# Performance work log

Hardware: AMD Instinct MI355X
Metric: run time of the kernel (lower is better)

## Reference

```python
import jax, jax.numpy as jnp
import numpy as np

# Module hyperparameters (match init_kwargs)
T0, Z0, T1, Z1, K, S, ROUTING = 4, 16, 8, 16, 5, 1, 3
PAD = 2  # hard-coded padding=2 in the torch module
N, H, W_SP = 4, 128, 128


def setup_inputs() -> dict:
    key = jax.random.key(0)
    k1, k2 = jax.random.split(key)
    u = jax.random.normal(k1, (N, T0, Z0, H, W_SP), dtype=jnp.float32)
    # t_0 independent Conv2d(z_0 -> t_1*z_1, k, s, padding=2, bias=False) weights
    W = jax.random.normal(k2, (T0, T1 * Z1, Z0, K, K), dtype=jnp.float32) * 0.05
    return {"u": u, "W": W}


def _squash(p):
    # squash along last (z_1) axis, matching torch: p_norm = sqrt(|p|^2 + 1e-9)
    n2 = jnp.sum(p * p, axis=-1, keepdims=True)
    n = jnp.sqrt(n2 + 1e-9)
    return n2 / (1.0 + n2) * p / n


def _capsule_convs(u, W):
    # t_0 independent convs == one grouped conv with feature_group_count=t_0
    n, t0, z0, h, w = u.shape
    x = u.reshape(n, t0 * z0, h, w)
    wk = W.reshape(t0 * T1 * Z1, z0, K, K)
    y = jax.lax.conv_general_dilated(
        x, wk, window_strides=(S, S), padding=[(PAD, PAD), (PAD, PAD)],
        dimension_numbers=("NCHW", "OIHW", "NCHW"), feature_group_count=t0)
    h1, w1 = y.shape[2], y.shape[3]
    # [N, t0*t1*z1, H1, W1] -> u_hat [t0, N, H1, W1, t1, z1]
    y = y.reshape(n, t0, T1, Z1, h1, w1)
    return jnp.transpose(y, (1, 0, 4, 5, 2, 3))


def _routing(u_hat):
    t0, n, h, w, t1, z1 = u_hat.shape
    dt = u_hat.dtype
    b = jnp.zeros((t0, n, t1, h, w), dt)  # NCHW layout per capsule type
    neg_inf = jnp.array(-jnp.inf, dt)
    zero = jnp.array(0.0, dt)
    win = (1, 1, 1, K, K)
    ones = (1, 1, 1, 1, 1)
    pad = [(0, 0), (0, 0), (0, 0), (PAD, PAD), (PAD, PAD)]
    v = None
    for d in range(ROUTING):
        uh = jax.lax.stop_gradient(u_hat) if d < ROUTING - 1 else u_hat
        # stability max: max_pool2d(k,1,pad=2) (pads with -inf) then max over t1
        b_max = jax.lax.reduce_window(b, neg_inf, jax.lax.max, win, ones, pad)
        b_max = jnp.max(b_max, axis=2, keepdims=True)
        c = jnp.exp(b - b_max)  # [t0, N, t1, H, W]
        # conv2d_same with ones kernel [1,t1,k,k] == channel-sum then kxk box-sum
        sum_c = jax.lax.reduce_window(jnp.sum(c, axis=2, keepdims=True), zero,
                                      jax.lax.add, win, ones, pad)
        r = c / sum_c                                   # [t0, N, t1, H, W]
        r = jnp.transpose(r, (0, 1, 3, 4, 2))[..., None]  # [t0,N,H,W,t1,1]
        p = jnp.sum(r * uh, axis=0)                     # [N, H, W, t1, z1]
        v = _squash(p)
        # NOTE: the original torch code computes b + (u_hat*v).sum(4) into a
        # list `b_t_list_` that is never assigned back, so b stays zero across
        # iterations. We faithfully reproduce that (no b update).
    return jnp.transpose(v, (0, 3, 4, 1, 2))  # [N, t1, z1, H, W]


def reference(u, W):
    return _routing(_capsule_convs(u, W))
```

## Files before the change

kernel.cpp:

```cpp
#include <hip/hip_runtime.h>
#include <hip/hip_bf16.h>


#define CO 128

typedef __attribute__((ext_vector_type(8))) short bf16x8;
typedef __attribute__((ext_vector_type(4))) float f32x4;

__device__ __forceinline__ void glds16(const void* g, void* l) {
    __builtin_amdgcn_global_load_lds((const __attribute__((address_space(1))) void*)g,
                                     (__attribute__((address_space(3))) void*)l, 16, 0, 0);
}

__global__ __launch_bounds__(256) void k_prep(const float* __restrict__ u,
                                              const float* __restrict__ Wsrc,
                                              ushort* __restrict__ ut,
                                              ushort* __restrict__ Wr2) {
    __shared__ float lt[64][65];
    int b = blockIdx.x;
    int t = threadIdx.x;
    if (b < 800) {
        int idx = b * 256 + t;
        int ci = idx & 63;
        int r  = idx >> 6;
        int co = r & 127;
        int kk = r >> 7;
        int t0 = ci >> 4, z0 = ci & 15;
        __hip_bfloat16 bb = __float2bfloat16(Wsrc[((t0 * CO + co) * 16 + z0) * 25 + kk]);
        int chunk = (ci >> 3) ^ (co & 7);
        Wr2[((kk * CO + co) << 6) + (chunk << 3) + (ci & 7)] = *(ushort*)&bb;
        return;
    }
    b -= 800;
    int wc = b & 1; int nh = b >> 1; int h = nh & 127; int n = nh >> 7;
    int w0 = wc * 64;
    int ciL = t >> 4;
    int wl  = (t & 15) * 4;
    const float* up = u + (size_t)n * (64 * 128 * 128) + h * 128 + w0;
#pragma unroll
    for (int p = 0; p < 4; ++p) {
        int ci = p * 16 + ciL;
        float4 v = *(const float4*)(up + (size_t)ci * 16384 + wl);
        lt[wl + 0][ci] = v.x;
        lt[wl + 1][ci] = v.y;
        lt[wl + 2][ci] = v.z;
        lt[wl + 3][ci] = v.w;
    }
    __syncthreads();
    ushort* op = ut + (((size_t)(n * 128 + h)) * 128 + w0) * 64;
#pragma unroll
    for (int p = 0; p < 2; ++p) {
        int item = p * 256 + t;
        int c8 = item & 7, w2 = item >> 3;
        bf16x8 vv;
#pragma unroll
        for (int j = 0; j < 8; ++j) {
            __hip_bfloat16 bb = __float2bfloat16(lt[w2][c8 * 8 + j]);
            vv[j] = *(ushort*)&bb;
        }
        *(bf16x8*)(op + (size_t)w2 * 64 + c8 * 8) = vv;
    }
}

__global__ __launch_bounds__(256) void k_caps(const ushort* __restrict__ ut,
                                              const ushort* __restrict__ Wr2,
                                              float* __restrict__ out) {
    __shared__ ushort As[240 * 80];
    __shared__ ushort Bs[2][128 * 64];

    int tid = threadIdx.x;
    int bid = blockIdx.x;
    int bx = bid & 7, by = (bid >> 3) & 15, n = bid >> 7;
    int h0 = by * 8, w0 = bx * 16;

    int lane = tid & 63, wid = tid >> 6;
    int wm4  = (wid >> 1) * 4;
    int wn64 = (wid & 1) * 64;
    int q = lane >> 4, m16 = lane & 15;
    int m7 = m16 & 7;

#pragma unroll
    for (int j = 0; j < 4; ++j) {
        int i = (j * 256 + wid * 64) * 8;
        glds16(Wr2 + (size_t)(i + lane * 8), &Bs[0][i]);
    }

    for (int i = tid; i < 1920; i += 256) {
        int p = i >> 3, c = i & 7;
        int rr = p / 20, cc = p - rr * 20;
        int hh = h0 + rr - 2, ww = w0 + cc - 2;
        bf16x8 v = {};
        if ((unsigned)hh < 128u && (unsigned)ww < 128u)
            v = *(const bf16x8*)(ut + (((size_t)(n * 128 + hh)) * 128 + ww) * 64 + c * 8);
        *(bf16x8*)&As[p * 80 + c * 8] = v;
    }
    __syncthreads();

    int aBase = (wm4 * 20 + m16) * 80 + q * 8;
    int bRow  = (wn64 + m16) << 6;

    f32x4 acc[4][4] = {};

#pragma unroll
    for (int kk = 0; kk < 25; ++kk) {
        const int kh = kk / 5, kw = kk % 5;
        const int cur = kk & 1;
        if (kk < 24) {
#pragma unroll
            for (int j = 0; j < 4; ++j) {
                int i = (j * 256 + wid * 64) * 8;
                glds16(Wr2 + (size_t)(kk + 1) * 8192 + i + lane * 8, &Bs[cur ^ 1][i]);
            }
        }
#pragma unroll
        for (int ks = 0; ks < 2; ++ks) {
            int sw = ((ks * 4 + q) ^ m7) << 3;
            bf16x8 a[4], bb[4];
#pragma unroll
            for (int mi = 0; mi < 4; ++mi)
                a[mi] = *(const bf16x8*)&As[aBase + ((mi + kh) * 20 + kw) * 80 + ks * 32];
#pragma unroll
            for (int ni = 0; ni < 4; ++ni)
                bb[ni] = *(const bf16x8*)&Bs[cur][bRow + ni * 1024 + sw];
#pragma unroll
            for (int mi = 0; mi < 4; ++mi)
#pragma unroll
                for (int ni = 0; ni < 4; ++ni)
                    acc[mi][ni] = __builtin_amdgcn_mfma_f32_16x16x32_bf16(
                        a[mi], bb[ni], acc[mi][ni], 0, 0, 0);
        }
        if (kk < 24) __syncthreads();
    }

#pragma unroll
    for (int mi = 0; mi < 4; ++mi) {
        int h = h0 + wm4 + mi;
        int hlo = h - 2; if (hlo < 0) hlo = 0;
        int hhi = h + 2; if (hhi > 127) hhi = 127;
        float cnth = (float)(hhi - hlo + 1);
#pragma unroll
        for (int ni = 0; ni < 4; ++ni) {
            f32x4 cv = acc[mi][ni];
            float ov[4];
#pragma unroll
            for (int reg = 0; reg < 4; ++reg) {
                int w = w0 + q * 4 + reg;
                int wlo = w - 2; if (wlo < 0) wlo = 0;
                int whi = w + 2; if (whi > 127) whi = 127;
                float s = 1.f / (8.f * cnth * (float)(whi - wlo + 1));
                float pv = cv[reg] * s;
                float n2 = pv * pv;
                n2 += __shfl_xor(n2, 1);
                n2 += __shfl_xor(n2, 2);
                n2 += __shfl_xor(n2, 4);
                n2 += __shfl_xor(n2, 8);
                float fac = n2 / ((1.f + n2) * sqrtf(n2 + 1e-9f));
                ov[reg] = pv * fac;
            }
            int co = wn64 + ni * 16 + m16;
            *(float4*)(out + (((size_t)(n * CO + co)) << 14) + h * 128 + w0 + q * 4) =
                make_float4(ov[0], ov[1], ov[2], ov[3]);
        }
    }
}

extern "C" void kernel_launch(void* const* d_in, const int* in_sizes, int n_in,
                              void* d_out, int out_size, void* d_ws, size_t ws_size,
                              hipStream_t stream) {
    const float* u    = (const float*)d_in[0];
    const float* Wsrc = (const float*)d_in[1];
    float* out = (float*)d_out;
    ushort* Wr2 = (ushort*)d_ws;
    ushort* ut  = (ushort*)((char*)d_ws + 409600);

    k_prep<<<1824, 256, 0, stream>>>(u, Wsrc, ut, Wr2);
    k_caps<<<512, 256, 0, stream>>>(ut, Wr2, out);
}
```

Measured before the change: 107.5 us.

## Fuse input transpose/bf16 conversion into conv kernel and triple-buffer weight tiles

Removes the separate pass that transposed u to channel-last bf16 in workspace. The conv kernel now gathers the fp32 halo tile directly from u, converts it to bf16 and stores it in an XOR-swizzled LDS layout with no padding. Weight staging moves from double to triple buffering, using explicit vmcnt waits and raw barriers plus setprio around the MFMA block. This saves a full read and write of the activations and a kernel's worth of work. In exchange, each thread issues 64 strided scalar fp32 loads when staging the halo tile, and the halo is re-read from global memory by neighbouring blocks.

```diff
diff --git a/kernel.cpp b/kernel.cpp
--- a/kernel.cpp
+++ b/kernel.cpp
@@ -12,61 +12,24 @@
                                      (__attribute__((address_space(3))) void*)l, 16, 0, 0);
 }
 
-__global__ __launch_bounds__(256) void k_prep(const float* __restrict__ u,
-                                              const float* __restrict__ Wsrc,
-                                              ushort* __restrict__ ut,
-                                              ushort* __restrict__ Wr2) {
-    __shared__ float lt[64][65];
-    int b = blockIdx.x;
-    int t = threadIdx.x;
-    if (b < 800) {
-        int idx = b * 256 + t;
-        int ci = idx & 63;
-        int r  = idx >> 6;
-        int co = r & 127;
-        int kk = r >> 7;
-        int t0 = ci >> 4, z0 = ci & 15;
-        __hip_bfloat16 bb = __float2bfloat16(Wsrc[((t0 * CO + co) * 16 + z0) * 25 + kk]);
-        int chunk = (ci >> 3) ^ (co & 7);
-        Wr2[((kk * CO + co) << 6) + (chunk << 3) + (ci & 7)] = *(ushort*)&bb;
-        return;
-    }
-    b -= 800;
-    int wc = b & 1; int nh = b >> 1; int h = nh & 127; int n = nh >> 7;
-    int w0 = wc * 64;
-    int ciL = t >> 4;
-    int wl  = (t & 15) * 4;
-    const float* up = u + (size_t)n * (64 * 128 * 128) + h * 128 + w0;
-#pragma unroll
-    for (int p = 0; p < 4; ++p) {
-        int ci = p * 16 + ciL;
-        float4 v = *(const float4*)(up + (size_t)ci * 16384 + wl);
-        lt[wl + 0][ci] = v.x;
-        lt[wl + 1][ci] = v.y;
-        lt[wl + 2][ci] = v.z;
-        lt[wl + 3][ci] = v.w;
-    }
-    __syncthreads();
-    ushort* op = ut + (((size_t)(n * 128 + h)) * 128 + w0) * 64;
-#pragma unroll
-    for (int p = 0; p < 2; ++p) {
-        int item = p * 256 + t;
-        int c8 = item & 7, w2 = item >> 3;
-        bf16x8 vv;
-#pragma unroll
-        for (int j = 0; j < 8; ++j) {
-            __hip_bfloat16 bb = __float2bfloat16(lt[w2][c8 * 8 + j]);
-            vv[j] = *(ushort*)&bb;
-        }
-        *(bf16x8*)(op + (size_t)w2 * 64 + c8 * 8) = vv;
-    }
+__global__ __launch_bounds__(256) void k_reorder(const float* __restrict__ Wsrc,
+                                                 ushort* __restrict__ Wr2) {
+    int idx = blockIdx.x * 256 + threadIdx.x;
+    int ci = idx & 63;
+    int r  = idx >> 6;
+    int co = r & 127;
+    int kk = r >> 7;
+    int t0 = ci >> 4, z0 = ci & 15;
+    __hip_bfloat16 bb = __float2bfloat16(Wsrc[((t0 * CO + co) * 16 + z0) * 25 + kk]);
+    int chunk = (ci >> 3) ^ (co & 7);
+    Wr2[((kk * CO + co) << 6) + (chunk << 3) + (ci & 7)] = *(ushort*)&bb;
 }
 
-__global__ __launch_bounds__(256) void k_caps(const ushort* __restrict__ ut,
+__global__ __launch_bounds__(256) void k_caps(const float* __restrict__ u,
                                               const ushort* __restrict__ Wr2,
                                               float* __restrict__ out) {
-    __shared__ ushort As[240 * 80];
-    __shared__ ushort Bs[2][128 * 64];
+    __shared__ ushort As[240 * 64];
+    __shared__ ushort Bs[3][128 * 64];
 
     int tid = threadIdx.x;
     int bid = blockIdx.x;
@@ -79,49 +42,68 @@
     int q = lane >> 4, m16 = lane & 15;
     int m7 = m16 & 7;
 
+    auto stageB = [&](int kk2, int buf) {
 #pragma unroll
-    for (int j = 0; j < 4; ++j) {
-        int i = (j * 256 + wid * 64) * 8;
-        glds16(Wr2 + (size_t)(i + lane * 8), &Bs[0][i]);
-    }
+        for (int j = 0; j < 4; ++j) {
+            int i = (j * 256 + wid * 64) * 8;
+            glds16(Wr2 + (size_t)kk2 * 8192 + i + lane * 8, &Bs[buf][i]);
+        }
+    };
 
-    for (int i = tid; i < 1920; i += 256) {
-        int p = i >> 3, c = i & 7;
-        int rr = p / 20, cc = p - rr * 20;
+    stageB(0, 0);
+
+    {
+        int p = tid;
+        int rr = p / 20;
+        int cc = p - rr * 20;
         int hh = h0 + rr - 2, ww = w0 + cc - 2;
-        bf16x8 v = {};
-        if ((unsigned)hh < 128u && (unsigned)ww < 128u)
-            v = *(const bf16x8*)(ut + (((size_t)(n * 128 + hh)) * 128 + ww) * 64 + c * 8);
-        *(bf16x8*)&As[p * 80 + c * 8] = v;
+        bool inb = (p < 240) & ((unsigned)hh < 128u) & ((unsigned)ww < 128u);
+        const float* up = u + (size_t)n * (64 * 128 * 128) + (size_t)hh * 128 + ww;
+        int key = (p & 7) << 3;
+#pragma unroll
+        for (int c8 = 0; c8 < 8; ++c8) {
+            bf16x8 vv = {};
+            if (inb) {
+#pragma unroll
+                for (int j = 0; j < 8; ++j) {
+                    __hip_bfloat16 bb =
+                        __float2bfloat16(up[(size_t)(c8 * 8 + j) * 16384]);
+                    vv[j] = *(ushort*)&bb;
+                }
+            }
+            if (p < 240)
+                *(bf16x8*)&As[(p << 6) + ((c8 << 3) ^ key)] = vv;
+        }
     }
     __syncthreads();
+    stageB(1, 1);
 
-    int aBase = (wm4 * 20 + m16) * 80 + q * 8;
-    int bRow  = (wn64 + m16) << 6;
+    int aP0  = wm4 * 20 + m16;
+    int bRow = (wn64 + m16) << 6;
+    int bsw0 = (q ^ m7) << 3;
+    int bsw1 = ((4 + q) ^ m7) << 3;
 
     f32x4 acc[4][4] = {};
 
 #pragma unroll
     for (int kk = 0; kk < 25; ++kk) {
         const int kh = kk / 5, kw = kk % 5;
-        const int cur = kk & 1;
-        if (kk < 24) {
-#pragma unroll
-            for (int j = 0; j < 4; ++j) {
-                int i = (j * 256 + wid * 64) * 8;
-                glds16(Wr2 + (size_t)(kk + 1) * 8192 + i + lane * 8, &Bs[cur ^ 1][i]);
-            }
-        }
+        const int cur = kk % 3;
+        if (kk < 23) stageB(kk + 2, (kk + 2) % 3);
+        __builtin_amdgcn_s_setprio(1);
 #pragma unroll
         for (int ks = 0; ks < 2; ++ks) {
-            int sw = ((ks * 4 + q) ^ m7) << 3;
+            int bsw = ks ? bsw1 : bsw0;
             bf16x8 a[4], bb[4];
 #pragma unroll
-            for (int mi = 0; mi < 4; ++mi)
-                a[mi] = *(const bf16x8*)&As[aBase + ((mi + kh) * 20 + kw) * 80 + ks * 32];
+            for (int mi = 0; mi < 4; ++mi) {
+                int p = aP0 + (mi + kh) * 20 + kw;
+                int asw = (((ks << 2) + q) ^ (p & 7)) << 3;
+                a[mi] = *(const bf16x8*)&As[(p << 6) + asw];
+            }
 #pragma unroll
             for (int ni = 0; ni < 4; ++ni)
-                bb[ni] = *(const bf16x8*)&Bs[cur][bRow + ni * 1024 + sw];
+                bb[ni] = *(const bf16x8*)&Bs[cur][bRow + ni * 1024 + bsw];
 #pragma unroll
             for (int mi = 0; mi < 4; ++mi)
 #pragma unroll
@@ -129,7 +111,12 @@
                     acc[mi][ni] = __builtin_amdgcn_mfma_f32_16x16x32_bf16(
                         a[mi], bb[ni], acc[mi][ni], 0, 0, 0);
         }
-        if (kk < 24) __syncthreads();
+        __builtin_amdgcn_s_setprio(0);
+        if (kk < 24) {
+            if (kk < 23) asm volatile("s_waitcnt vmcnt(4)" ::: "memory");
+            else         asm volatile("s_waitcnt vmcnt(0)" ::: "memory");
+            asm volatile("s_barrier" ::: "memory");
+        }
     }
 
 #pragma unroll
@@ -171,8 +158,7 @@
     const float* Wsrc = (const float*)d_in[1];
     float* out = (float*)d_out;
     ushort* Wr2 = (ushort*)d_ws;
-    ushort* ut  = (ushort*)((char*)d_ws + 409600);
 
-    k_prep<<<1824, 256, 0, stream>>>(u, Wsrc, ut, Wr2);
-    k_caps<<<512, 256, 0, stream>>>(ut, Wr2, out);
+    k_reorder<<<800, 256, 0, stream>>>(Wsrc, Wr2);
+    k_caps<<<512, 256, 0, stream>>>(u, Wr2, out);
 }
```

New measurement: 107.2 us. About the same (-0.3%).

## Triple-buffer weight tiles with split prefetch and explicit barriers in capsule conv

Applied to the files above, without the earlier changes.

Replaces the double-buffered B tile with a three-stage ring that prefetches two kernel taps ahead, issued in halves interleaved with each k-substep. Synchronisation moves from __syncthreads to explicit s_barrier with vmcnt/lgkmcnt waits, sched_barrier and setprio around the MFMA block, so global-to-LDS loads overlap compute. The A tile row stride shrinks from 80 to 68 elements, which changes LDS bank mapping and footprint. The hand-tuned waitcnt counts carry correctness risk if the vmcnt accounting is wrong.

```diff
diff --git a/kernel.cpp b/kernel.cpp
--- a/kernel.cpp
+++ b/kernel.cpp
@@ -65,8 +65,8 @@
 __global__ __launch_bounds__(256) void k_caps(const ushort* __restrict__ ut,
                                               const ushort* __restrict__ Wr2,
                                               float* __restrict__ out) {
-    __shared__ ushort As[240 * 80];
-    __shared__ ushort Bs[2][128 * 64];
+    __shared__ ushort As[240 * 68];
+    __shared__ ushort Bs[3 * 128 * 64];
 
     int tid = threadIdx.x;
     int bid = blockIdx.x;
@@ -74,63 +74,84 @@
     int h0 = by * 8, w0 = bx * 16;
 
     int lane = tid & 63, wid = tid >> 6;
-    int wm4  = (wid >> 1) * 4;
-    int wn64 = (wid & 1) * 64;
+    int rg = wid >> 1;
+    int cg = wid & 1;
+    int wm4  = rg * 4;
+    int wn64 = cg * 64;
     int q = lane >> 4, m16 = lane & 15;
     int m7 = m16 & 7;
 
-#pragma unroll
-    for (int j = 0; j < 4; ++j) {
-        int i = (j * 256 + wid * 64) * 8;
-        glds16(Wr2 + (size_t)(i + lane * 8), &Bs[0][i]);
+#define STAGEB_HALF(kk2, bufOfs, half)                                      \
+    {                                                                       \
+        _Pragma("unroll") for (int j_ = (half) * 2; j_ < (half) * 2 + 2; ++j_) { \
+            int i_ = (j_ * 256 + wid * 64) * 8;                             \
+            glds16(Wr2 + (size_t)(kk2) * 8192 + i_ + lane * 8,              \
+                   &Bs[(bufOfs) + i_]);                                     \
+        }                                                                   \
     }
+
+    STAGEB_HALF(0, 0, 0);
+    STAGEB_HALF(0, 0, 1);
 
     for (int i = tid; i < 1920; i += 256) {
         int p = i >> 3, c = i & 7;
         int rr = p / 20, cc = p - rr * 20;
         int hh = h0 + rr - 2, ww = w0 + cc - 2;
         bf16x8 v = {};
-        if ((unsigned)hh < 128u && (unsigned)ww < 128u)
+        if (((unsigned)hh < 128u) & ((unsigned)ww < 128u))
             v = *(const bf16x8*)(ut + (((size_t)(n * 128 + hh)) * 128 + ww) * 64 + c * 8);
-        *(bf16x8*)&As[p * 80 + c * 8] = v;
+        *(bf16x8*)&As[p * 68 + c * 8] = v;
     }
     __syncthreads();
+    STAGEB_HALF(1, 8192, 0);
+    STAGEB_HALF(1, 8192, 1);
 
-    int aBase = (wm4 * 20 + m16) * 80 + q * 8;
+    const ushort* ap = As + (wm4 * 20 + m16) * 68 + q * 8;
     int bRow  = (wn64 + m16) << 6;
+    int bsw0  = (q ^ m7) << 3;
+    int bsw1  = ((4 + q) ^ m7) << 3;
 
     f32x4 acc[4][4] = {};
 
 #pragma unroll
     for (int kk = 0; kk < 25; ++kk) {
         const int kh = kk / 5, kw = kk % 5;
-        const int cur = kk & 1;
-        if (kk < 24) {
-#pragma unroll
-            for (int j = 0; j < 4; ++j) {
-                int i = (j * 256 + wid * 64) * 8;
-                glds16(Wr2 + (size_t)(kk + 1) * 8192 + i + lane * 8, &Bs[cur ^ 1][i]);
-            }
-        }
+        const int cur = (kk % 3) * 8192;
+        const int nxt = ((kk + 2) % 3) * 8192;
 #pragma unroll
         for (int ks = 0; ks < 2; ++ks) {
-            int sw = ((ks * 4 + q) ^ m7) << 3;
             bf16x8 a[4], bb[4];
+            const int bsw = ks ? bsw1 : bsw0;
 #pragma unroll
             for (int mi = 0; mi < 4; ++mi)
-                a[mi] = *(const bf16x8*)&As[aBase + ((mi + kh) * 20 + kw) * 80 + ks * 32];
+                a[mi] = *(const bf16x8*)(ap + ((mi + kh) * 20 + kw) * 68 + ks * 32);
 #pragma unroll
             for (int ni = 0; ni < 4; ++ni)
-                bb[ni] = *(const bf16x8*)&Bs[cur][bRow + ni * 1024 + sw];
+                bb[ni] = *(const bf16x8*)&Bs[cur + bRow + ni * 1024 + bsw];
+            if (kk < 23) STAGEB_HALF(kk + 2, nxt, ks);
+            __builtin_amdgcn_s_barrier();
+            asm volatile("s_waitcnt lgkmcnt(0)" ::: "memory");
+            __builtin_amdgcn_sched_barrier(0);
+            __builtin_amdgcn_s_setprio(1);
 #pragma unroll
             for (int mi = 0; mi < 4; ++mi)
 #pragma unroll
                 for (int ni = 0; ni < 4; ++ni)
                     acc[mi][ni] = __builtin_amdgcn_mfma_f32_16x16x32_bf16(
                         a[mi], bb[ni], acc[mi][ni], 0, 0, 0);
+            __builtin_amdgcn_s_setprio(0);
+            if (ks == 0) {
+                __builtin_amdgcn_s_barrier();
+            } else if (kk < 23) {
+                asm volatile("s_waitcnt vmcnt(4)" ::: "memory");
+                __builtin_amdgcn_s_barrier();
+            } else if (kk == 23) {
+                asm volatile("s_waitcnt vmcnt(0)" ::: "memory");
+                __builtin_amdgcn_s_barrier();
+            }
         }
-        if (kk < 24) __syncthreads();
     }
+#undef STAGEB_HALF
 
 #pragma unroll
     for (int mi = 0; mi < 4; ++mi) {
```

Result: slower. 140.0 us (+30.2%).
